# Optimization experiments

Measured on AMD Instinct MI355X. Metric: run time of the kernel, lower is better.

Reference implementation:

```python
import jax, jax.numpy as jnp
import numpy as np

V_IN = 32000   # len_input (input vocab)
V_OUT = 32000  # len_output (output vocab)
E = 1024       # num_embedd
H = 1024       # hidden
L = 2          # num_layer
B = 32         # batch
S = 128        # source seq len
T = 64         # target seq len


def setup_inputs() -> dict:
    key = jax.random.key(0)
    ks = jax.random.split(key, 16)
    p = lambda k, shape: jax.random.normal(k, shape, dtype=jnp.float32) * 0.02
    return {
        "input_tokens": jax.random.randint(ks[0], (B, S), 0, V_IN, dtype=jnp.int32),
        "target": jax.random.randint(ks[1], (B, T), 0, V_OUT, dtype=jnp.int32),
        "tf_mask": jax.random.randint(ks[2], (T,), 0, 2, dtype=jnp.int32),
        "in_emb": p(ks[3], (V_IN, E)),
        "out_emb": p(ks[4], (V_OUT, E)),
        "enc_Wih": p(ks[5], (L, 4 * H, E)),
        "enc_Whh": p(ks[6], (L, 4 * H, H)),
        "enc_bih": p(ks[7], (L, 4 * H)),
        "enc_bhh": p(ks[8], (L, 4 * H)),
        "dec_Wih": p(ks[9], (L, 4 * H, E)),
        "dec_Whh": p(ks[10], (L, 4 * H, H)),
        "dec_bih": p(ks[11], (L, 4 * H)),
        "dec_bhh": p(ks[12], (L, 4 * H)),
        "W_out": p(ks[13], (V_OUT, H)),
        "b_out": p(ks[14], (V_OUT,)),
    }


def _lstm_cell(x, h, c, Wih, Whh, bih, bhh):
    # PyTorch gate order: input, forget, cell(g), output
    gates = x @ Wih.T + h @ Whh.T + bih + bhh  # [B, 4H]
    i, f, g, o = jnp.split(gates, 4, axis=-1)
    c_new = jax.nn.sigmoid(f) * c + jax.nn.sigmoid(i) * jnp.tanh(g)
    h_new = jax.nn.sigmoid(o) * jnp.tanh(c_new)
    return h_new, c_new


def reference(input_tokens, target, tf_mask, in_emb, out_emb,
              enc_Wih, enc_Whh, enc_bih, enc_bhh,
              dec_Wih, dec_Whh, dec_bih, dec_bhh,
              W_out, b_out):
    batch, tgt_len = target.shape
    hid = enc_Whh.shape[-1]
    n_layers = enc_Wih.shape[0]
    dtype = in_emb.dtype

    # ---- Encoder: multi-layer LSTM over the full source sequence ----
    seq = in_emb[input_tokens]  # [B, S, E]
    h0 = jnp.zeros((batch, hid), dtype)
    h_list, c_list = [], []
    for l in range(n_layers):
        Wih, Whh, bih, bhh = enc_Wih[l], enc_Whh[l], enc_bih[l], enc_bhh[l]
        def step(carry, xt):
            h, c = carry
            h, c = _lstm_cell(xt, h, c, Wih, Whh, bih, bhh)
            return (h, c), h
        (hT, cT), ys = jax.lax.scan(step, (h0, h0), seq.swapaxes(0, 1))
        seq = ys.swapaxes(0, 1)  # [B, S, H] feeds next layer
        h_list.append(hT)
        c_list.append(cT)
    h = jnp.stack(h_list)  # [L, B, H]
    c = jnp.stack(c_list)  # [L, B, H]

    # ---- Decoder: one token at a time with teacher forcing ----
    def dec_step(carry, xs):
        h, c, tok = carry
        tgt_t, tf_t = xs
        x = out_emb[tok]  # [B, E]
        new_h, new_c = [], []
        for l in range(n_layers):
            hl, cl = _lstm_cell(x, h[l], c[l], dec_Wih[l], dec_Whh[l],
                                dec_bih[l], dec_bhh[l])
            new_h.append(hl)
            new_c.append(cl)
            x = hl
        pred = x @ W_out.T + b_out  # [B, V_OUT]
        top1 = jnp.argmax(pred, axis=-1).astype(tok.dtype)
        next_tok = jnp.where(tf_t > 0, tgt_t, top1)
        return (jnp.stack(new_h), jnp.stack(new_c), next_tok), pred

    xs = (target[:, 1:].swapaxes(0, 1), tf_mask[1:])  # steps t = 1..T-1
    _, preds = jax.lax.scan(dec_step, (h, c, target[:, 0]), xs)
    # outputs[:, 0] stays zero, matching the torch module
    outputs = jnp.concatenate(
        [jnp.zeros((batch, 1, W_out.shape[0]), dtype), preds.swapaxes(0, 1)],
        axis=1)
    return outputs
```

## Files before the change

### kernel.cpp

```cpp
#include <hip/hip_runtime.h>
#include <cstdint>

#define S_  128
#define Tt_ 64
#define V_  32000
#define NB_ 256

typedef _Float16 h8 __attribute__((ext_vector_type(8)));
typedef float    f4 __attribute__((ext_vector_type(4)));

#define MFMA16(a,b,c) __builtin_amdgcn_mfma_f32_16x16x32_f16((a),(b),(c),0,0,0)

__device__ __forceinline__ void split8p(const float* __restrict__ p, h8& hi, h8& lo) {
  f4 a = *(const f4*)p;
  f4 b = *(const f4*)(p + 4);
#pragma unroll
  for (int i = 0; i < 4; i++) {
    _Float16 h0 = (_Float16)a[i];
    hi[i] = h0; lo[i] = (_Float16)((a[i] - (float)h0) * 2048.0f);
    _Float16 h1 = (_Float16)b[i];
    hi[i+4] = h1; lo[i+4] = (_Float16)((b[i] - (float)h1) * 2048.0f);
  }
}

__device__ __forceinline__ void gsync(unsigned* flags, unsigned target) {
  asm volatile("s_waitcnt vmcnt(0)" ::: "memory");
  __syncthreads();
  int tid = threadIdx.x;
  if (tid == 0) {
    __hip_atomic_store(&flags[blockIdx.x * 4], target, __ATOMIC_RELAXED,
                       __HIP_MEMORY_SCOPE_AGENT);
  }
  if (tid < 64) {
    bool done;
    do {
      unsigned m = 0xFFFFFFFFu;
#pragma unroll
      for (int q = 0; q < 4; ++q) {
        unsigned f = __hip_atomic_load(&flags[(tid + q * 64) * 4], __ATOMIC_RELAXED,
                                       __HIP_MEMORY_SCOPE_AGENT);
        m = m < f ? m : f;
      }
      done = (bool)__all(m >= target);
      if (!done) __builtin_amdgcn_s_sleep(1);
    } while (!done);
  }
  __builtin_amdgcn_sched_barrier(0);
  __syncthreads();
  asm volatile("" ::: "memory");
}

__device__ __forceinline__ void store_h_pair(_Float16* __restrict__ oH,
                                             _Float16* __restrict__ oL,
                                             int b, int col0, int lane,
                                             _Float16 hh, _Float16 hl) {
  unsigned hs = (unsigned)__builtin_bit_cast(unsigned short, hh);
  unsigned ls = (unsigned)__builtin_bit_cast(unsigned short, hl);
  unsigned ph = (unsigned)__shfl_xor((int)hs, 32, 64);
  unsigned pl = (unsigned)__shfl_xor((int)ls, 32, 64);
  if (lane < 32) {
    unsigned hw = hs | (ph << 16);
    __hip_atomic_store((unsigned*)(oH + (size_t)b * 1024 + col0), hw,
                       __ATOMIC_RELAXED, __HIP_MEMORY_SCOPE_AGENT);
  } else {
    unsigned lw = pl | (ls << 16);
    __hip_atomic_store((unsigned*)(oL + (size_t)b * 1024 + col0), lw,
                       __ATOMIC_RELAXED, __HIP_MEMORY_SCOPE_AGENT);
  }
}


__global__ void k_prep0(float* __restrict__ out,
                        _Float16* __restrict__ seqH, _Float16* __restrict__ seqL,
                        _Float16* __restrict__ ehH, _Float16* __restrict__ ehL,
                        unsigned* __restrict__ encF, unsigned* __restrict__ decF) {
  int stride = gridDim.x * 256;
  for (unsigned idx = blockIdx.x * 256 + threadIdx.x; idx < 32u * V_; idx += stride) {
    unsigned b = idx / V_, v = idx - b * V_;
    out[(size_t)b * (Tt_ * V_) + v] = 0.0f;
  }
  for (unsigned idx = blockIdx.x * 256 + threadIdx.x; idx < 16384; idx += stride) {
    ((unsigned*)seqH)[idx] = 0u; ((unsigned*)seqL)[idx] = 0u;
    ((unsigned*)ehH)[idx]  = 0u; ((unsigned*)ehL)[idx]  = 0u;
  }
  for (unsigned idx = blockIdx.x * 256 + threadIdx.x; idx < NB_ * 4; idx += stride) {
    encF[idx] = 0u; decF[idx] = 0u;
  }
}

__global__ void k_dw2(const float* __restrict__ decWih, const float* __restrict__ decWhh,
                      _Float16* __restrict__ W2H, _Float16* __restrict__ W2L) {
  int b = blockIdx.x;
  int l = b >> 12, rem = b & 4095;
  int blk = rem >> 4, w = rem & 15;
  int t = threadIdx.x;
  int ks = t >> 6, lane = t & 63;
  int j16 = lane & 15;
  int grow = (j16 >> 2) * 1024 + blk * 4 + (j16 & 3);
  int kk = w * 128 + ks * 32 + (lane >> 4) * 8;
  const float* src = (kk < 1024)
      ? decWih + ((size_t)l * 4096 + grow) * 1024 + kk
      : decWhh + ((size_t)l * 4096 + grow) * 1024 + (kk - 1024);
  h8 hi, lo; split8p(src, hi, lo);
  size_t d = ((((size_t)l * 256 + blk) * 16 + w) * 4 + ks) * 512 + lane * 8;
  *(h8*)(W2H + d) = hi;
  *(h8*)(W2L + d) = lo;
}

__global__ void k_ew1(const float* __restrict__ encWih, const float* __restrict__ encWhh,
                      _Float16* __restrict__ W1H, _Float16* __restrict__ W1L) {
  int b = blockIdx.x;
  int blk = b >> 4, rem = b & 15;
  int ws = rem >> 2, ksq = rem & 3;
  int t = threadIdx.x;
  int ks = ksq * 4 + (t >> 6), lane = t & 63;
  int j16 = lane & 15;
  int grow = (j16 >> 2) * 1024 + blk * 4 + (j16 & 3);
  int kk = ws * 512 + ks * 32 + (lane >> 4) * 8;
  const float* src = (kk < 1024)
      ? encWih + ((size_t)4096 + grow) * 1024 + kk
      : encWhh + ((size_t)4096 + grow) * 1024 + (kk - 1024);
  h8 hi, lo; split8p(src, hi, lo);
  size_t d = (((size_t)(blk * 4 + ws)) * 16 + ks) * 512 + lane * 8;
  *(h8*)(W1H + d) = hi;
  *(h8*)(W1L + d) = lo;
}

__global__ void k_wo2(const float* __restrict__ Wout,
                      _Float16* __restrict__ Wo2H, _Float16* __restrict__ Wo2L) {
  int b = blockIdx.x;
  int vt = b >> 3, kb = (b & 7) * 4;
  int t = threadIdx.x;
  int ks = kb + (t >> 6), lane = t & 63;
  int vcol = vt * 16 + (lane & 15);
  int kk = ks * 32 + (lane >> 4) * 8;
  h8 hi, lo; split8p(Wout + (size_t)vcol * 1024 + kk, hi, lo);
  size_t d = ((size_t)vt * 32 + ks) * 512 + lane * 8;
  *(h8*)(Wo2H + d) = hi;
  *(h8*)(Wo2L + d) = lo;
}

__global__ void k_emb(const int* __restrict__ itoks, const float* __restrict__ in_emb,
                      _Float16* __restrict__ embH, _Float16* __restrict__ embL) {
  int n = blockIdx.x;
  int b = n & 31, t = n >> 5;
  int tok = itoks[b * S_ + t];
  int k = threadIdx.x * 8;
  h8 hi, lo;
  split8p(in_emb + (size_t)tok * 1024 + k, hi, lo);
  *(h8*)(embH + (size_t)n * 1024 + k) = hi;
  *(h8*)(embL + (size_t)n * 1024 + k) = lo;
}


struct EP {
  const float* encWih; const float* encWhh; const float* encbih; const float* encbhh;
  const _Float16 *W1H, *W1L;
  const _Float16 *embH, *embL;
  _Float16 *seqH, *seqL;
  _Float16 *ehH, *ehL;
  _Float16 *h0s0H, *h0s0L;
  _Float16 *h1s0H, *h1s0L;
  float *cb0, *cb1;
  unsigned* flags;
};

__device__ __forceinline__ int wadr(int row, int k) {
  return row * 2048 + ((((k << 1) ^ ((row & 7) << 4))) >> 1);
}

__device__ void preload_enc(const float* __restrict__ Wih, const float* __restrict__ Whh,
                            int blk, int tid, _Float16* sWH, _Float16* sWL) {
#pragma unroll 4
  for (int it = 0; it < 16; ++it) {
    int lin = (it * 512 + tid) * 4;
    int j16 = lin >> 11;
    int k   = lin & 2047;
    int g = j16 >> 2, u = j16 & 3;
    int grow = g * 1024 + blk * 4 + u;
    const float* src = (k < 1024) ? (Wih + (size_t)grow * 1024 + k)
                                  : (Whh + (size_t)grow * 1024 + (k - 1024));
    f4 x = *(const f4*)src;
#pragma unroll
    for (int q = 0; q < 4; q++) {
      _Float16 hh = (_Float16)x[q];
      sWH[wadr(j16, k + q)] = hh;
      sWL[wadr(j16, k + q)] = (_Float16)((x[q] - (float)hh) * 2048.0f);
    }
  }
}

__device__ void gates_enc(const _Float16* sWH, const _Float16* sWL, float* sScr,
                          const _Float16* __restrict__ xH, const _Float16* __restrict__ xL,
                          const _Float16* __restrict__ hHb, const _Float16* __restrict__ hLb,
                          int tid) {
  int w = tid >> 6, lane = tid & 63;
  int kbase = w * 512;
  bool xp = (w < 2);
  int j16 = lane & 15;
  const _Float16* aH = xp ? xH : (hHb - 1024);
  const _Float16* aL = xp ? xL : (hLb - 1024);
  f4 accH[2] = {}, accM[2] = {};
#pragma unroll
  for (int kc = 0; kc < 4; ++kc) {
    h8 Ah[4][2], Al[4][2];
#pragma unroll
    for (int k4 = 0; k4 < 4; ++k4) {
      int kk = kbase + (kc * 4 + k4) * 32 + (lane >> 4) * 8;
#pragma unroll
      for (int mt = 0; mt < 2; ++mt) {
        int brow = mt * 16 + (lane & 15);
        Ah[k4][mt] = *(const h8*)(aH + (size_t)brow * 1024 + kk);
        Al[k4][mt] = *(const h8*)(aL + (size_t)brow * 1024 + kk);
      }
    }
#pragma unroll
    for (int k4 = 0; k4 < 4; ++k4) {
      int kk = kbase + (kc * 4 + k4) * 32 + (lane >> 4) * 8;
      h8 Bh = *(const h8*)(sWH + wadr(j16, kk));
      h8 Bl = *(const h8*)(sWL + wadr(j16, kk));
#pragma unroll
      for (int mt = 0; mt < 2; ++mt) {
        accH[mt] = MFMA16(Ah[k4][mt], Bh, accH[mt]);
        accM[mt] = MFMA16(Ah[k4][mt], Bl, accM[mt]);
        accM[mt] = MFMA16(Al[k4][mt], Bh, accM[mt]);
      }
    }
  }
#pragma unroll
  for (int mt = 0; mt < 2; ++mt)
#pragma unroll
    for (int r = 0; r < 4; ++r) {
      int b = mt * 16 + (lane >> 4) * 4 + r;
      sScr[w * 544 + b * 17 + j16] = accH[mt][r] + accM[mt][r] * (1.0f / 2048.0f);
    }
}

__device__ void gates_enc1(const _Float16* __restrict__ W1H, const _Float16* __restrict__ W1L,
                           float* sScr,
                           const _Float16* __restrict__ xH, const _Float16* __restrict__ xL,
                           const _Float16* __restrict__ hHb, const _Float16* __restrict__ hLb,
                           int blk, int tid) {
  int w = tid >> 6, lane = tid & 63;
  int ws = w - 4;
  int kbase = ws * 512;
  bool xp = (ws < 2);
  int j16 = lane & 15;
  const _Float16* aH = xp ? xH : (hHb - 1024);
  const _Float16* aL = xp ? xL : (hLb - 1024);
  const _Float16* bH = W1H + (((size_t)(blk * 4 + ws)) * 16) * 512 + lane * 8;
  const _Float16* bL = W1L + (((size_t)(blk * 4 + ws)) * 16) * 512 + lane * 8;
  f4 accH[2] = {}, accM[2] = {};
#pragma unroll
  for (int kc = 0; kc < 4; ++kc) {
    h8 Bh[4], Bl[4], Ah[4][2], Al[4][2];
#pragma unroll
    for (int k4 = 0; k4 < 4; ++k4) {
      int ks = kc * 4 + k4;
      Bh[k4] = *(const h8*)(bH + ks * 512);
      Bl[k4] = *(const h8*)(bL + ks * 512);
      int kk = kbase + ks * 32 + (lane >> 4) * 8;
#pragma unroll
      for (int mt = 0; mt < 2; ++mt) {
        int brow = mt * 16 + (lane & 15);
        Ah[k4][mt] = *(const h8*)(aH + (size_t)brow * 1024 + kk);
        Al[k4][mt] = *(const h8*)(aL + (size_t)brow * 1024 + kk);
      }
    }
#pragma unroll
    for (int k4 = 0; k4 < 4; ++k4)
#pragma unroll
      for (int mt = 0; mt < 2; ++mt) {
        accH[mt] = MFMA16(Ah[k4][mt], Bh[k4], accH[mt]);
        accM[mt] = MFMA16(Ah[k4][mt], Bl[k4], accM[mt]);
        accM[mt] = MFMA16(Al[k4][mt], Bh[k4], accM[mt]);
      }
  }
#pragma unroll
  for (int mt = 0; mt < 2; ++mt)
#pragma unroll
    for (int r = 0; r < 4; ++r) {
      int b = mt * 16 + (lane >> 4) * 4 + r;
      sScr[w * 544 + b * 17 + j16] = accH[mt][r] + accM[mt][r] * (1.0f / 2048.0f);
    }
}

__device__ void finish_enc(float* sScr, int blk, int tid,
                           const float* __restrict__ bih, const float* __restrict__ bhh,
                           float& c,
                           _Float16* __restrict__ oH, _Float16* __restrict__ oL,
                           _Float16* __restrict__ oH2, _Float16* __restrict__ oL2,
                           float* __restrict__ cOut) {
  if (tid >= 0 && tid < 128) {
    int u = tid >> 5, b = tid & 31, lane = tid & 63;
    float g[4];
#pragma unroll
    for (int gg = 0; gg < 4; ++gg) {
      int j = gg * 4 + u;
      float s = sScr[0 * 544 + b * 17 + j] + sScr[1 * 544 + b * 17 + j]
              + sScr[2 * 544 + b * 17 + j] + sScr[3 * 544 + b * 17 + j];
      int grow = gg * 1024 + blk * 4 + u;
      g[gg] = s + bih[grow] + bhh[grow];
    }
    float ii = 1.0f / (1.0f + expf(-g[0]));
    float ff = 1.0f / (1.0f + expf(-g[1]));
    float gt = tanhf(g[2]);
    float oo = 1.0f / (1.0f + expf(-g[3]));
    c = ff * c + ii * gt;
    float hn = oo * tanhf(c);
    _Float16 hh = (_Float16)hn;
    _Float16 hl = (_Float16)((hn - (float)hh) * 2048.0f);
    int col0 = blk * 4 + (u & 2);
    store_h_pair(oH, oL, b, col0, lane, hh, hl);
    size_t ci = (size_t)b * 1024 + blk * 4 + u;
    if (oH2) { oH2[ci] = hh; oL2[ci] = hl; }
    if (cOut) cOut[ci] = c;
  }
}

__global__ void __launch_bounds__(512, 2) voice_enc(EP P) {
  __shared__ _Float16 sWH[16 * 2048];
  __shared__ _Float16 sWL[16 * 2048];
  __shared__ float    sScr[8 * 544];
  int blk = blockIdx.x, tid = threadIdx.x;
  int w = tid >> 6;
  float cA = 0.0f, cB = 0.0f;
  unsigned ep = 0;

  preload_enc(P.encWih, P.encWhh, blk, tid, sWH, sWL);
  __syncthreads();

  for (int t = 0; t <= 128; ++t) {
    if (w < 4) {
      if (t < 128)
        gates_enc(sWH, sWL, sScr,
                  P.embH + (size_t)t * 32768, P.embL + (size_t)t * 32768,
                  P.seqH + (size_t)t * 32768, P.seqL + (size_t)t * 32768, tid);
    } else {
      if (t >= 1)
        gates_enc1(P.W1H, P.W1L, sScr,
                   P.seqH + (size_t)t * 32768, P.seqL + (size_t)t * 32768,
                   P.ehH + (size_t)(t - 1) * 32768, P.ehL + (size_t)(t - 1) * 32768,
                   blk, tid);
    }
    __syncthreads();
    if (t < 128 && tid < 256) {
      bool last = (t == 127);
      finish_enc(sScr, blk, tid, P.encbih, P.encbhh, cA,
                 P.seqH + (size_t)(t + 1) * 32768, P.seqL + (size_t)(t + 1) * 32768,
                 last ? P.h0s0H : nullptr, last ? P.h0s0L : nullptr,
                 last ? P.cb0 : nullptr);
    }
    if (t >= 1 && tid >= 256) {
      bool last = (t == 128);
      finish_enc(sScr + 4 * 544, blk, tid - 256, P.encbih + 4096, P.encbhh + 4096, cB,
                 P.ehH + (size_t)t * 32768, P.ehL + (size_t)t * 32768,
                 last ? P.h1s0H : nullptr, last ? P.h1s0L : nullptr,
                 last ? P.cb1 : nullptr);
    }
    gsync(P.flags, ++ep * NB_);
  }
}


struct DP {
  const float* out_emb; const int* target; const int* tfm;
  const _Float16 *dW2H, *dW2L;
  const float *decbih, *decbhh;
  const _Float16 *Wo2H, *Wo2L;
  const float* bout;
  _Float16 *hist0H, *hist0L;
  _Float16 *hist1H, *hist1L;
  const float *cb0, *cb1;
  unsigned long long* amax;
  unsigned* flags;
};

template <int XM>
__device__ void dcell16(const _Float16* __restrict__ W2H, const _Float16* __restrict__ W2L,
                        const _Float16* __restrict__ xH, const _Float16* __restrict__ xL,
                        const float* __restrict__ out_emb, int tok0, int tok1,
                        const _Float16* __restrict__ hH, const _Float16* __restrict__ hL,
                        float* sScr, int blk, int tid) {
  int w = tid >> 6, lane = tid & 63;
  int j16 = lane & 15;
  int kbase = w * 128;
  bool xp = (w < 8);
  const _Float16* aH = xp ? xH : (hH - 1024);
  const _Float16* aL = xp ? xL : (hL - 1024);
  const _Float16* wbH = W2H + (((size_t)(blk * 16 + w)) * 4) * 512 + lane * 8;
  const _Float16* wbL = W2L + (((size_t)(blk * 16 + w)) * 4) * 512 + lane * 8;
  h8 Bh[4], Bl[4];
#pragma unroll
  for (int ks = 0; ks < 4; ++ks) {
    Bh[ks] = *(const h8*)(wbH + ks * 512);
    Bl[ks] = *(const h8*)(wbL + ks * 512);
  }
  f4 accH[2] = {}, accM[2] = {};
#pragma unroll
  for (int kc = 0; kc < 2; ++kc) {
    h8 Ah[2][2], Al[2][2];
#pragma unroll
    for (int k2 = 0; k2 < 2; ++k2) {
      int kk = kbase + (kc * 2 + k2) * 32 + (lane >> 4) * 8;
#pragma unroll
      for (int mt = 0; mt < 2; ++mt) {
        int brow = mt * 16 + j16;
        if (XM == 2 && xp) {
          int tk = mt ? tok1 : tok0;
          split8p(out_emb + (size_t)tk * 1024 + kk, Ah[k2][mt], Al[k2][mt]);
        } else {
          Ah[k2][mt] = *(const h8*)(aH + (size_t)brow * 1024 + kk);
          Al[k2][mt] = *(const h8*)(aL + (size_t)brow * 1024 + kk);
        }
      }
    }
#pragma unroll
    for (int k2 = 0; k2 < 2; ++k2) {
      int ks = kc * 2 + k2;
#pragma unroll
      for (int mt = 0; mt < 2; ++mt) {
        accH[mt] = MFMA16(Ah[k2][mt], Bh[ks], accH[mt]);
        accM[mt] = MFMA16(Ah[k2][mt], Bl[ks], accM[mt]);
        accM[mt] = MFMA16(Al[k2][mt], Bh[ks], accM[mt]);
      }
    }
  }
#pragma unroll
  for (int mt = 0; mt < 2; ++mt)
#pragma unroll
    for (int r = 0; r < 4; ++r) {
      int b = mt * 16 + (lane >> 4) * 4 + r;
      sScr[w * 544 + b * 17 + j16] = accH[mt][r] + accM[mt][r] * (1.0f / 2048.0f);
    }
}

__device__ void dcell_finish16(float* sScr, int blk, int tid,
                               const float* __restrict__ bih, const float* __restrict__ bhh,
                               float& c,
                               _Float16* __restrict__ oH, _Float16* __restrict__ oL) {
  __syncthreads();
  if (tid < 128) {
    int u = tid >> 5, b = tid & 31, lanef = tid & 63;
    float g[4];
#pragma unroll
    for (int gg = 0; gg < 4; ++gg) {
      int j = gg * 4 + u;
      float s = 0.0f;
#pragma unroll
      for (int ww = 0; ww < 16; ++ww) s += sScr[ww * 544 + b * 17 + j];
      int growf = gg * 1024 + blk * 4 + u;
      g[gg] = s + bih[growf] + bhh[growf];
    }
    float ii = 1.0f / (1.0f + expf(-g[0]));
    float ff = 1.0f / (1.0f + expf(-g[1]));
    float gt = tanhf(g[2]);
    float oo = 1.0f / (1.0f + expf(-g[3]));
    c = ff * c + ii * gt;
    float hn = oo * tanhf(c);
    _Float16 hh = (_Float16)hn;
    _Float16 hl = (_Float16)((hn - (float)hh) * 2048.0f);
    int col0 = blk * 4 + (u & 2);
    store_h_pair(oH, oL, b, col0, lanef, hh, hl);
  }
}

__global__ void __launch_bounds__(1024, 4) voice_dec(DP P) {
  __shared__ float sScr[16 * 544];
  int blk = blockIdx.x, tid = threadIdx.x;
  int w = tid >> 6, lane = tid & 63;
  unsigned ep = 0;
  float c0 = 0.0f, c1 = 0.0f;
  if (tid < 128) {
    int u = tid >> 5, b = tid & 31;
    size_t ci = (size_t)b * 1024 + blk * 4 + u;
    c0 = P.cb0[ci];
    c1 = P.cb1[ci];
  }
  const _Float16* W0H = P.dW2H;
  const _Float16* W0L = P.dW2L;
  const _Float16* W1H = P.dW2H + (size_t)8388608;
  const _Float16* W1L = P.dW2L + (size_t)8388608;

  for (int i = 0; i < 63; ++i) {
    _Float16* h0in   = P.hist0H + (size_t)i * 32768;       _Float16* h0inL  = P.hist0L + (size_t)i * 32768;
    _Float16* h0out  = P.hist0H + (size_t)(i + 1) * 32768; _Float16* h0outL = P.hist0L + (size_t)(i + 1) * 32768;
    _Float16* h1in   = P.hist1H + (size_t)i * 32768;       _Float16* h1inL  = P.hist1L + (size_t)i * 32768;
    _Float16* h1out  = P.hist1H + (size_t)(i + 1) * 32768; _Float16* h1outL = P.hist1L + (size_t)(i + 1) * 32768;

    int tok0 = 0, tok1 = 0;
    if (w < 8) {
      int b0 = lane & 15, b1 = 16 + (lane & 15);
      if (i == 0)              { tok0 = P.target[b0 * Tt_];     tok1 = P.target[b1 * Tt_]; }
      else if (P.tfm[i] > 0)   { tok0 = P.target[b0 * Tt_ + i]; tok1 = P.target[b1 * Tt_ + i]; }
      else {
        unsigned long long a0 = __hip_atomic_load(&P.amax[b0], __ATOMIC_RELAXED, __HIP_MEMORY_SCOPE_AGENT);
        unsigned long long a1 = __hip_atomic_load(&P.amax[b1], __ATOMIC_RELAXED, __HIP_MEMORY_SCOPE_AGENT);
        tok0 = (int)(~(unsigned)a0); tok1 = (int)(~(unsigned)a1);
      }
    }
    dcell16<2>(W0H, W0L, nullptr, nullptr, P.out_emb, tok0, tok1,
               h0in, h0inL, sScr, blk, tid);
    dcell_finish16(sScr, blk, tid, P.decbih, P.decbhh, c0, h0out, h0outL);
    gsync(P.flags, ++ep * NB_);

    if (blk == 0 && tid < 32)
      __hip_atomic_store(&P.amax[tid], 0ull, __ATOMIC_RELAXED, __HIP_MEMORY_SCOPE_AGENT);
    dcell16<0>(W1H, W1L, h0out, h0outL, nullptr, 0, 0,
               h1in, h1inL, sScr, blk, tid);
    dcell_finish16(sScr, blk, tid, P.decbih + 4096, P.decbhh + 4096, c1, h1out, h1outL);
    gsync(P.flags, ++ep * NB_);

    bool needC = (i < 62) && (P.tfm[i + 1] == 0);
    if (needC) {
      int vt = blk * 8 + (w >> 1);
      int kh = w & 1;
      if (vt < 2000) {
        const _Float16* bH = P.Wo2H + ((size_t)vt * 32 + kh * 16) * 512 + lane * 8;
        const _Float16* bL = P.Wo2L + ((size_t)vt * 32 + kh * 16) * 512 + lane * 8;
        int kof = (lane >> 4) * 8;
        f4 accH[2] = {}, accM[2] = {};
#pragma unroll
        for (int kc = 0; kc < 4; ++kc) {
          h8 Bh[4], Bl[4], Ah[4][2], Al[4][2];
#pragma unroll
          for (int k4 = 0; k4 < 4; ++k4) {
            int ks = kc * 4 + k4;
            Bh[k4] = __builtin_nontemporal_load((const h8*)(bH + ks * 512));
            Bl[k4] = __builtin_nontemporal_load((const h8*)(bL + ks * 512));
            int kk = (kh * 16 + ks) * 32 + kof;
#pragma unroll
            for (int mt = 0; mt < 2; ++mt) {
              int brow = mt * 16 + (lane & 15);
              Ah[k4][mt] = *(const h8*)(h1out  + (size_t)brow * 1024 + kk);
              Al[k4][mt] = *(const h8*)(h1outL + (size_t)brow * 1024 + kk);
            }
          }
#pragma unroll
          for (int k4 = 0; k4 < 4; ++k4)
#pragma unroll
            for (int mt = 0; mt < 2; ++mt) {
              accH[mt] = MFMA16(Ah[k4][mt], Bh[k4], accH[mt]);
              accM[mt] = MFMA16(Ah[k4][mt], Bl[k4], accM[mt]);
              accM[mt] = MFMA16(Al[k4][mt], Bh[k4], accM[mt]);
            }
        }
#pragma unroll
        for (int mt = 0; mt < 2; ++mt)
#pragma unroll
          for (int r = 0; r < 4; ++r)
            sScr[w * 512 + (mt * 4 + r) * 64 + lane] =
                accH[mt][r] + accM[mt][r] * (1.0f / 2048.0f);
      }
      __syncthreads();
      if (vt < 2000 && kh == 0) {
        float biasv = P.bout[vt * 16 + (lane & 15)];
#pragma unroll
        for (int mt = 0; mt < 2; ++mt) {
          float vr[4];
#pragma unroll
          for (int r = 0; r < 4; ++r) {
            int idx = (mt * 4 + r) * 64 + lane;
            vr[r] = sScr[w * 512 + idx] + sScr[(w + 1) * 512 + idx] + biasv;
          }
#pragma unroll
          for (int r = 0; r < 4; ++r) {
            float v = vr[r];
            unsigned id = (unsigned)(vt * 16 + (lane & 15));
#pragma unroll
            for (int off = 1; off < 16; off <<= 1) {
              float ov = __shfl_xor(v, off, 64);
              unsigned oi = __shfl_xor(id, off, 64);
              if (ov > v || (ov == v && oi < id)) { v = ov; id = oi; }
            }
            if ((lane & 15) == 0) {
              unsigned kb = __float_as_uint(v);
              kb = (kb & 0x80000000u) ? ~kb : (kb | 0x80000000u);
              unsigned long long key = ((unsigned long long)kb << 32) | (unsigned)(~id);
              int b = mt * 16 + (lane >> 4) * 4 + r;
              unsigned long long cur = __hip_atomic_load(&P.amax[b], __ATOMIC_RELAXED,
                                                         __HIP_MEMORY_SCOPE_AGENT);
              if (cur < key) atomicMax(&P.amax[b], key);
            }
          }
        }
      }
      gsync(P.flags, ++ep * NB_);
    }
  }
}

__global__ void __launch_bounds__(256, 2)
k_out(const _Float16* __restrict__ histH, const _Float16* __restrict__ histL,
      const _Float16* __restrict__ Wo2H, const _Float16* __restrict__ Wo2L,
      const float* __restrict__ bout, float* __restrict__ out) {
  int bid = blockIdx.x;
  int nb = bid / 16, mg = bid % 16;
  int w = threadIdx.x >> 6, lane = threadIdx.x & 63;
  int kof = (lane >> 4) * 8;
  int mt0 = mg * 8 + w * 2;
  f4 accH[2][4] = {}, accM[2][4] = {};
  for (int ks = 0; ks < 32; ++ks) {
    int kk = ks * 32 + kof;
    h8 Ah[2], Al[2];
#pragma unroll
    for (int mti = 0; mti < 2; ++mti) {
      int mt = mt0 + mti;
      if (mt < 126) {
        int m = mt * 16 + (lane & 15);
        int ii = m >> 5, b = m & 31;
        size_t ai = (size_t)(ii + 1) * 32768 + (size_t)b * 1024 + kk;
        Ah[mti] = *(const h8*)(histH + ai);
        Al[mti] = *(const h8*)(histL + ai);
      }
    }
#pragma unroll
    for (int nt = 0; nt < 4; ++nt) {
      size_t bi = ((size_t)(nb * 4 + nt) * 32 + ks) * 512 + lane * 8;
      h8 Bh = __builtin_nontemporal_load((const h8*)(Wo2H + bi));
      h8 Bl = __builtin_nontemporal_load((const h8*)(Wo2L + bi));
#pragma unroll
      for (int mti = 0; mti < 2; ++mti) {
        if (mt0 + mti < 126) {
          accH[mti][nt] = MFMA16(Ah[mti], Bh, accH[mti][nt]);
          accM[mti][nt] = MFMA16(Ah[mti], Bl, accM[mti][nt]);
          accM[mti][nt] = MFMA16(Al[mti], Bh, accM[mti][nt]);
        }
      }
    }
  }
#pragma unroll
  for (int mti = 0; mti < 2; ++mti) {
    int mt = mt0 + mti;
    if (mt >= 126) continue;
#pragma unroll
    for (int nt = 0; nt < 4; ++nt) {
      int vcol = (nb * 4 + nt) * 16 + (lane & 15);
      float bias = bout[vcol];
#pragma unroll
      for (int r = 0; r < 4; ++r) {
        int m = mt * 16 + (lane >> 4) * 4 + r;
        int ii = m >> 5, b = m & 31;
        out[(size_t)b * (Tt_ * V_) + (size_t)(ii + 1) * V_ + vcol] =
            accH[mti][nt][r] + accM[mti][nt][r] * (1.0f / 2048.0f) + bias;
      }
    }
  }
}


extern "C" void kernel_launch(void* const* d_in, const int* in_sizes, int n_in,
                              void* d_out, int out_size, void* d_ws, size_t ws_size,
                              hipStream_t stream) {
  const int*   itoks   = (const int*)d_in[0];
  const int*   target  = (const int*)d_in[1];
  const int*   tfm     = (const int*)d_in[2];
  const float* in_emb  = (const float*)d_in[3];
  const float* out_emb = (const float*)d_in[4];
  const float* encWih  = (const float*)d_in[5];
  const float* encWhh  = (const float*)d_in[6];
  const float* encbih  = (const float*)d_in[7];
  const float* encbhh  = (const float*)d_in[8];
  const float* decWih  = (const float*)d_in[9];
  const float* decWhh  = (const float*)d_in[10];
  const float* decbih  = (const float*)d_in[11];
  const float* decbhh  = (const float*)d_in[12];
  const float* Wout    = (const float*)d_in[13];
  const float* bout    = (const float*)d_in[14];
  float* out = (float*)d_out;

  char* ws = (char*)d_ws;
  size_t off = 0;
  auto alloc = [&](size_t bytes) { void* p = ws + off; off += (bytes + 255) & ~(size_t)255; return p; };
  _Float16* seqH  = (_Float16*)alloc((size_t)129 * 32768 * 2);
  _Float16* seqL  = (_Float16*)alloc((size_t)129 * 32768 * 2);
  _Float16* ehH   = (_Float16*)alloc((size_t)129 * 32768 * 2);
  _Float16* ehL   = (_Float16*)alloc((size_t)129 * 32768 * 2);
  _Float16* embH  = (_Float16*)alloc((size_t)128 * 32768 * 2);
  _Float16* embL  = (_Float16*)alloc((size_t)128 * 32768 * 2);
  _Float16* hist0H = (_Float16*)alloc((size_t)64 * 32768 * 2);
  _Float16* hist0L = (_Float16*)alloc((size_t)64 * 32768 * 2);
  _Float16* hist1H = (_Float16*)alloc((size_t)64 * 32768 * 2);
  _Float16* hist1L = (_Float16*)alloc((size_t)64 * 32768 * 2);
  float*    cb0   = (float*)alloc((size_t)32 * 1024 * 4);
  float*    cb1   = (float*)alloc((size_t)32 * 1024 * 4);
  _Float16* dW2H  = (_Float16*)alloc((size_t)2 * 8388608 * 2);
  _Float16* dW2L  = (_Float16*)alloc((size_t)2 * 8388608 * 2);
  _Float16* W1eH  = (_Float16*)alloc((size_t)1024 * 16 * 512 * 2);
  _Float16* W1eL  = (_Float16*)alloc((size_t)1024 * 16 * 512 * 2);
  _Float16* Wo2H  = (_Float16*)alloc((size_t)2000 * 32 * 512 * 2);
  _Float16* Wo2L  = (_Float16*)alloc((size_t)2000 * 32 * 512 * 2);
  unsigned long long* amax = (unsigned long long*)alloc(32 * 8);
  unsigned* encF = (unsigned*)alloc(NB_ * 4 * 4);
  unsigned* decF = (unsigned*)alloc(NB_ * 4 * 4);
  if (off > ws_size) return;

  k_prep0<<<1024, 256, 0, stream>>>(out, seqH, seqL, ehH, ehL, encF, decF);
  k_dw2<<<8192, 256, 0, stream>>>(decWih, decWhh, dW2H, dW2L);
  k_ew1<<<4096, 256, 0, stream>>>(encWih, encWhh, W1eH, W1eL);
  k_wo2<<<16000, 256, 0, stream>>>(Wout, Wo2H, Wo2L);
  k_emb<<<4096, 128, 0, stream>>>(itoks, in_emb, embH, embL);

  EP E;
  E.encWih = encWih; E.encWhh = encWhh; E.encbih = encbih; E.encbhh = encbhh;
  E.W1H = W1eH; E.W1L = W1eL;
  E.embH = embH; E.embL = embL;
  E.seqH = seqH; E.seqL = seqL; E.ehH = ehH; E.ehL = ehL;
  E.h0s0H = hist0H; E.h0s0L = hist0L; E.h1s0H = hist1H; E.h1s0L = hist1L;
  E.cb0 = cb0; E.cb1 = cb1; E.flags = encF;
  void* eargs[] = { &E };
  hipLaunchCooperativeKernel((void*)voice_enc, dim3(NB_), dim3(512), eargs, 0, stream);

  DP D;
  D.out_emb = out_emb; D.target = target; D.tfm = tfm;
  D.dW2H = dW2H; D.dW2L = dW2L; D.decbih = decbih; D.decbhh = decbhh;
  D.Wo2H = Wo2H; D.Wo2L = Wo2L; D.bout = bout;
  D.hist0H = hist0H; D.hist0L = hist0L; D.hist1H = hist1H; D.hist1L = hist1L;
  D.cb0 = cb0; D.cb1 = cb1; D.amax = amax; D.flags = decF;
  void* dargs[] = { &D };
  hipLaunchCooperativeKernel((void*)voice_dec, dim3(NB_), dim3(1024), dargs, 0, stream);

  k_out<<<8000, 256, 0, stream>>>(hist1H, hist1L, Wo2H, Wo2L, bout, out);
}
```

Baseline: 7.993 ms.

## Keep layer-1 encoder and decoder LSTM weight slices resident in registers

The encoder's layer-1 weight fragments (16 h8 hi/lo pairs per lane) and both decoder layers' weight fragments are now loaded into registers once, before the time loop, instead of being re-read from global memory every timestep. This removes repeated weight traffic on the latency-critical recurrent path. The decoder cell and output projection loops are also restructured to interleave loads and MFMAs with smaller live arrays. The cost is much higher register pressure, which under the 512x2 launch bounds may cause spills or reduce overlap of loads.

```diff
diff --git a/kernel.cpp b/kernel.cpp
--- a/kernel.cpp
+++ b/kernel.cpp
@@ -236,11 +236,11 @@
     }
 }
 
-__device__ void gates_enc1(const _Float16* __restrict__ W1H, const _Float16* __restrict__ W1L,
+__device__ __forceinline__ void gates_enc1(const h8 (&WrH)[16], const h8 (&WrL)[16],
                            float* sScr,
                            const _Float16* __restrict__ xH, const _Float16* __restrict__ xL,
                            const _Float16* __restrict__ hHb, const _Float16* __restrict__ hLb,
-                           int blk, int tid) {
+                           int tid) {
   int w = tid >> 6, lane = tid & 63;
   int ws = w - 4;
   int kbase = ws * 512;
@@ -248,18 +248,13 @@
   int j16 = lane & 15;
   const _Float16* aH = xp ? xH : (hHb - 1024);
   const _Float16* aL = xp ? xL : (hLb - 1024);
-  const _Float16* bH = W1H + (((size_t)(blk * 4 + ws)) * 16) * 512 + lane * 8;
-  const _Float16* bL = W1L + (((size_t)(blk * 4 + ws)) * 16) * 512 + lane * 8;
   f4 accH[2] = {}, accM[2] = {};
 #pragma unroll
   for (int kc = 0; kc < 4; ++kc) {
-    h8 Bh[4], Bl[4], Ah[4][2], Al[4][2];
+    h8 Ah[4][2], Al[4][2];
 #pragma unroll
     for (int k4 = 0; k4 < 4; ++k4) {
-      int ks = kc * 4 + k4;
-      Bh[k4] = *(const h8*)(bH + ks * 512);
-      Bl[k4] = *(const h8*)(bL + ks * 512);
-      int kk = kbase + ks * 32 + (lane >> 4) * 8;
+      int kk = kbase + (kc * 4 + k4) * 32 + (lane >> 4) * 8;
 #pragma unroll
       for (int mt = 0; mt < 2; ++mt) {
         int brow = mt * 16 + (lane & 15);
@@ -268,13 +263,15 @@
       }
     }
 #pragma unroll
-    for (int k4 = 0; k4 < 4; ++k4)
+    for (int k4 = 0; k4 < 4; ++k4) {
+      int ks = kc * 4 + k4;
 #pragma unroll
       for (int mt = 0; mt < 2; ++mt) {
-        accH[mt] = MFMA16(Ah[k4][mt], Bh[k4], accH[mt]);
-        accM[mt] = MFMA16(Ah[k4][mt], Bl[k4], accM[mt]);
-        accM[mt] = MFMA16(Al[k4][mt], Bh[k4], accM[mt]);
-      }
+        accH[mt] = MFMA16(Ah[k4][mt], WrH[ks], accH[mt]);
+        accM[mt] = MFMA16(Ah[k4][mt], WrL[ks], accM[mt]);
+        accM[mt] = MFMA16(Al[k4][mt], WrH[ks], accM[mt]);
+      }
+    }
   }
 #pragma unroll
   for (int mt = 0; mt < 2; ++mt)
@@ -323,9 +320,21 @@
   __shared__ _Float16 sWL[16 * 2048];
   __shared__ float    sScr[8 * 544];
   int blk = blockIdx.x, tid = threadIdx.x;
-  int w = tid >> 6;
+  int w = tid >> 6, lane = tid & 63;
   float cA = 0.0f, cB = 0.0f;
   unsigned ep = 0;
+
+  h8 w1rh[16], w1rl[16];
+  if (w >= 4) {
+    int ws = w - 4;
+    const _Float16* bH = P.W1H + (((size_t)(blk * 4 + ws)) * 16) * 512 + lane * 8;
+    const _Float16* bL = P.W1L + (((size_t)(blk * 4 + ws)) * 16) * 512 + lane * 8;
+#pragma unroll
+    for (int ks = 0; ks < 16; ++ks) {
+      w1rh[ks] = *(const h8*)(bH + ks * 512);
+      w1rl[ks] = *(const h8*)(bL + ks * 512);
+    }
+  }
 
   preload_enc(P.encWih, P.encWhh, blk, tid, sWH, sWL);
   __syncthreads();
@@ -338,10 +347,10 @@
                   P.seqH + (size_t)t * 32768, P.seqL + (size_t)t * 32768, tid);
     } else {
       if (t >= 1)
-        gates_enc1(P.W1H, P.W1L, sScr,
+        gates_enc1(w1rh, w1rl, sScr,
                    P.seqH + (size_t)t * 32768, P.seqL + (size_t)t * 32768,
                    P.ehH + (size_t)(t - 1) * 32768, P.ehL + (size_t)(t - 1) * 32768,
-                   blk, tid);
+                   tid);
     }
     __syncthreads();
     if (t < 128 && tid < 256) {
@@ -377,53 +386,35 @@
 };
 
 template <int XM>
-__device__ void dcell16(const _Float16* __restrict__ W2H, const _Float16* __restrict__ W2L,
-                        const _Float16* __restrict__ xH, const _Float16* __restrict__ xL,
-                        const float* __restrict__ out_emb, int tok0, int tok1,
-                        const _Float16* __restrict__ hH, const _Float16* __restrict__ hL,
-                        float* sScr, int blk, int tid) {
+__device__ __forceinline__ void dcell16r(const h8 (&Bh)[4], const h8 (&Bl)[4],
+                      const _Float16* __restrict__ xH, const _Float16* __restrict__ xL,
+                      const float* __restrict__ out_emb, int tok0, int tok1,
+                      const _Float16* __restrict__ hH, const _Float16* __restrict__ hL,
+                      float* sScr, int blk, int tid) {
   int w = tid >> 6, lane = tid & 63;
   int j16 = lane & 15;
   int kbase = w * 128;
   bool xp = (w < 8);
   const _Float16* aH = xp ? xH : (hH - 1024);
   const _Float16* aL = xp ? xL : (hL - 1024);
-  const _Float16* wbH = W2H + (((size_t)(blk * 16 + w)) * 4) * 512 + lane * 8;
-  const _Float16* wbL = W2L + (((size_t)(blk * 16 + w)) * 4) * 512 + lane * 8;
-  h8 Bh[4], Bl[4];
-#pragma unroll
-  for (int ks = 0; ks < 4; ++ks) {
-    Bh[ks] = *(const h8*)(wbH + ks * 512);
-    Bl[ks] = *(const h8*)(wbL + ks * 512);
-  }
   f4 accH[2] = {}, accM[2] = {};
 #pragma unroll
-  for (int kc = 0; kc < 2; ++kc) {
-    h8 Ah[2][2], Al[2][2];
-#pragma unroll
-    for (int k2 = 0; k2 < 2; ++k2) {
-      int kk = kbase + (kc * 2 + k2) * 32 + (lane >> 4) * 8;
-#pragma unroll
-      for (int mt = 0; mt < 2; ++mt) {
-        int brow = mt * 16 + j16;
-        if (XM == 2 && xp) {
-          int tk = mt ? tok1 : tok0;
-          split8p(out_emb + (size_t)tk * 1024 + kk, Ah[k2][mt], Al[k2][mt]);
-        } else {
-          Ah[k2][mt] = *(const h8*)(aH + (size_t)brow * 1024 + kk);
-          Al[k2][mt] = *(const h8*)(aL + (size_t)brow * 1024 + kk);
-        }
-      }
-    }
-#pragma unroll
-    for (int k2 = 0; k2 < 2; ++k2) {
-      int ks = kc * 2 + k2;
-#pragma unroll
-      for (int mt = 0; mt < 2; ++mt) {
-        accH[mt] = MFMA16(Ah[k2][mt], Bh[ks], accH[mt]);
-        accM[mt] = MFMA16(Ah[k2][mt], Bl[ks], accM[mt]);
-        accM[mt] = MFMA16(Al[k2][mt], Bh[ks], accM[mt]);
-      }
+  for (int mt = 0; mt < 2; ++mt) {
+    int brow = mt * 16 + j16;
+    int tk = mt ? tok1 : tok0;
+#pragma unroll
+    for (int ks = 0; ks < 4; ++ks) {
+      int kk = kbase + ks * 32 + (lane >> 4) * 8;
+      h8 Ah, Al;
+      if (XM == 2 && xp) {
+        split8p(out_emb + (size_t)tk * 1024 + kk, Ah, Al);
+      } else {
+        Ah = *(const h8*)(aH + (size_t)brow * 1024 + kk);
+        Al = *(const h8*)(aL + (size_t)brow * 1024 + kk);
+      }
+      accH[mt] = MFMA16(Ah, Bh[ks], accH[mt]);
+      accM[mt] = MFMA16(Ah, Bl[ks], accM[mt]);
+      accM[mt] = MFMA16(Al, Bh[ks], accM[mt]);
     }
   }
 #pragma unroll
@@ -470,6 +461,19 @@
   int blk = blockIdx.x, tid = threadIdx.x;
   int w = tid >> 6, lane = tid & 63;
   unsigned ep = 0;
+
+  h8 w0h[4], w0l[4], w1h[4], w1l[4];
+  {
+    size_t woff = (((size_t)(blk * 16 + w)) * 4) * 512 + lane * 8;
+#pragma unroll
+    for (int ks = 0; ks < 4; ++ks) {
+      w0h[ks] = *(const h8*)(P.dW2H + woff + (size_t)ks * 512);
+      w0l[ks] = *(const h8*)(P.dW2L + woff + (size_t)ks * 512);
+      w1h[ks] = *(const h8*)(P.dW2H + (size_t)8388608 + woff + (size_t)ks * 512);
+      w1l[ks] = *(const h8*)(P.dW2L + (size_t)8388608 + woff + (size_t)ks * 512);
+    }
+  }
+
   float c0 = 0.0f, c1 = 0.0f;
   if (tid < 128) {
     int u = tid >> 5, b = tid & 31;
@@ -477,10 +481,6 @@
     c0 = P.cb0[ci];
     c1 = P.cb1[ci];
   }
-  const _Float16* W0H = P.dW2H;
-  const _Float16* W0L = P.dW2L;
-  const _Float16* W1H = P.dW2H + (size_t)8388608;
-  const _Float16* W1L = P.dW2L + (size_t)8388608;
 
   for (int i = 0; i < 63; ++i) {
     _Float16* h0in   = P.hist0H + (size_t)i * 32768;       _Float16* h0inL  = P.hist0L + (size_t)i * 32768;
@@ -499,15 +499,15 @@
         tok0 = (int)(~(unsigned)a0); tok1 = (int)(~(unsigned)a1);
       }
     }
-    dcell16<2>(W0H, W0L, nullptr, nullptr, P.out_emb, tok0, tok1,
-               h0in, h0inL, sScr, blk, tid);
+    dcell16r<2>(w0h, w0l, nullptr, nullptr, P.out_emb, tok0, tok1,
+                h0in, h0inL, sScr, blk, tid);
     dcell_finish16(sScr, blk, tid, P.decbih, P.decbhh, c0, h0out, h0outL);
     gsync(P.flags, ++ep * NB_);
 
     if (blk == 0 && tid < 32)
       __hip_atomic_store(&P.amax[tid], 0ull, __ATOMIC_RELAXED, __HIP_MEMORY_SCOPE_AGENT);
-    dcell16<0>(W1H, W1L, h0out, h0outL, nullptr, 0, 0,
-               h1in, h1inL, sScr, blk, tid);
+    dcell16r<0>(w1h, w1l, h0out, h0outL, nullptr, 0, 0,
+                h1in, h1inL, sScr, blk, tid);
     dcell_finish16(sScr, blk, tid, P.decbih + 4096, P.decbhh + 4096, c1, h1out, h1outL);
     gsync(P.flags, ++ep * NB_);
 
@@ -521,29 +521,19 @@
         int kof = (lane >> 4) * 8;
         f4 accH[2] = {}, accM[2] = {};
 #pragma unroll
-        for (int kc = 0; kc < 4; ++kc) {
-          h8 Bh[4], Bl[4], Ah[4][2], Al[4][2];
-#pragma unroll
-          for (int k4 = 0; k4 < 4; ++k4) {
-            int ks = kc * 4 + k4;
-            Bh[k4] = __builtin_nontemporal_load((const h8*)(bH + ks * 512));
-            Bl[k4] = __builtin_nontemporal_load((const h8*)(bL + ks * 512));
-            int kk = (kh * 16 + ks) * 32 + kof;
-#pragma unroll
-            for (int mt = 0; mt < 2; ++mt) {
-              int brow = mt * 16 + (lane & 15);
-              Ah[k4][mt] = *(const h8*)(h1out  + (size_t)brow * 1024 + kk);
-              Al[k4][mt] = *(const h8*)(h1outL + (size_t)brow * 1024 + kk);
-            }
+        for (int ks = 0; ks < 16; ++ks) {
+          h8 Bh = __builtin_nontemporal_load((const h8*)(bH + ks * 512));
+          h8 Bl = __builtin_nontemporal_load((const h8*)(bL + ks * 512));
+          int kk = (kh * 16 + ks) * 32 + kof;
+#pragma unroll
+          for (int mt = 0; mt < 2; ++mt) {
+            int brow = mt * 16 + (lane & 15);
+            h8 Ah = *(const h8*)(h1out  + (size_t)brow * 1024 + kk);
+            h8 Al = *(const h8*)(h1outL + (size_t)brow * 1024 + kk);
+            accH[mt] = MFMA16(Ah, Bh, accH[mt]);
+            accM[mt] = MFMA16(Ah, Bl, accM[mt]);
+            accM[mt] = MFMA16(Al, Bh, accM[mt]);
           }
-#pragma unroll
-          for (int k4 = 0; k4 < 4; ++k4)
-#pragma unroll
-            for (int mt = 0; mt < 2; ++mt) {
-              accH[mt] = MFMA16(Ah[k4][mt], Bh[k4], accH[mt]);
-              accM[mt] = MFMA16(Ah[k4][mt], Bl[k4], accM[mt]);
-              accM[mt] = MFMA16(Al[k4][mt], Bh[k4], accM[mt]);
-            }
         }
 #pragma unroll
         for (int mt = 0; mt < 2; ++mt)
```

Result: slower. 10.23 ms (+28.0%).
